# Kernel optimization log

Measured on AMD Instinct MI355X. Metric: run time of the kernel, lower is better.

Reference implementation:

```python
import jax, jax.numpy as jnp
import numpy as np


def setup_inputs() -> dict:
    key = jax.random.key(0)
    k1, k2, k3, k4, k5 = jax.random.split(key, 5)
    B, S, H, L = 32, 4096, 512, 2
    scale = 1.0 / np.sqrt(H)
    return {
        "out": jax.random.normal(k1, (B, S, H), dtype=jnp.float32),
        "hidden": jax.random.normal(k2, (L, B, H), dtype=jnp.float32),
        "W": jax.random.normal(k3, (H, H), dtype=jnp.float32) * scale,
        "b": jax.random.normal(k4, (H,), dtype=jnp.float32) * scale,
        "v": jax.random.normal(k5, (H,), dtype=jnp.float32) * scale,
    }


def reference(out, hidden, W, b, v):
    # hidden_last: (B, 1, H) from last layer
    h_last = hidden[-1][:, None, :]
    # energy = tanh(out @ W^T + b + h_last)  -> (B, S, H)
    energy = jnp.tanh(jnp.einsum("bsh,oh->bso", out, W) + b + h_last)
    # scores = energy @ v  -> (B, S)
    scores = jnp.einsum("bsh,h->bs", energy, v)
    attn = jax.nn.softmax(scores, axis=-1)
    # context = sum_s attn[b,s] * out[b,s,:]  -> (B, H)
    context = jnp.einsum("bs,bsh->bh", attn, out)
    return (context, attn)
```

## Files before the change

kernel.cpp:

```cpp
#include <hip/hip_runtime.h>
#include <hip/hip_bf16.h>

#define B_ 32
#define S_ 4096
#define H_ 512
#define M_ (B_ * S_)
#define L_ 2

typedef __bf16 bf16;
typedef bf16 bf16x8 __attribute__((ext_vector_type(8)));
typedef bf16 bf16x4 __attribute__((ext_vector_type(4)));
typedef float floatx4 __attribute__((ext_vector_type(4)));

__device__ inline bf16 f2b(float f) { return (bf16)f; }

__device__ inline float fast_tanh(float x) {
    float xc = fminf(15.0f, fmaxf(-15.0f, x));
    float e = __expf(2.0f * xc);
    return (e - 1.0f) * __builtin_amdgcn_rcpf(e + 1.0f);
}

__global__ __launch_bounds__(256) void convert_W(const float* __restrict__ W,
                                                 bf16* __restrict__ Wb) {
    int i = blockIdx.x * 256 + threadIdx.x;
    float4 w = ((const float4*)W)[i];
    bf16x4 p = { f2b(w.x), f2b(w.y), f2b(w.z), f2b(w.w) };
    *(bf16x4*)(Wb + (size_t)i * 4) = p;
}

#define MT 64
#define ASTRIDE 520
#define WSTRIDE 40

__global__ __launch_bounds__(256, 2) void scores_kernel(
    const float* __restrict__ outT,
    const bf16*  __restrict__ Wb,
    const float* __restrict__ bias,
    const float* __restrict__ hidden,
    const float* __restrict__ v,
    float* __restrict__ scores)
{
    __shared__ bf16 Alds[MT * ASTRIDE];
    __shared__ bf16 Wlds[128 * WSTRIDE];

    const int tid   = threadIdx.x;
    const int wave  = tid >> 6;
    const int lane  = tid & 63;
    const int mhalf = wave >> 1;
    const int nhalf = wave & 1;
    const int q     = lane >> 4;
    const int l16   = lane & 15;

    const int m0    = blockIdx.x * MT;
    const int batch = m0 >> 12;

    {
        const float4* src = (const float4*)(outT + (size_t)m0 * H_);
        #pragma unroll 4
        for (int it = 0; it < 32; ++it) {
            int idx = it * 256 + tid;
            int r   = idx >> 7;
            int c4  = idx & 127;
            float4 f = src[idx];
            bf16x4 p = { f2b(f.x), f2b(f.y), f2b(f.z), f2b(f.w) };
            *(bf16x4*)&Alds[r * ASTRIDE + c4 * 4] = p;
        }
    }

    float score_acc[2][4];
    #pragma unroll
    for (int mt = 0; mt < 2; ++mt)
        #pragma unroll
        for (int r = 0; r < 4; ++r) score_acc[mt][r] = 0.0f;

    const int nwbase = nhalf * 64;

    for (int nb = 0; nb < 4; ++nb) {
        floatx4 acc[2][4];
        #pragma unroll
        for (int mt = 0; mt < 2; ++mt)
            #pragma unroll
            for (int nt = 0; nt < 4; ++nt)
                acc[mt][nt] = (floatx4){0.f, 0.f, 0.f, 0.f};

        for (int kc = 0; kc < 16; ++kc) {
            __syncthreads();
            {
                int r    = tid >> 1;
                int hcol = tid & 1;
                const bf16* gsrc = Wb + (size_t)(nb * 128 + r) * H_ + kc * 32 + hcol * 16;
                uint4 u0 = *(const uint4*)(gsrc);
                uint4 u1 = *(const uint4*)(gsrc + 8);
                bf16* dst = &Wlds[r * WSTRIDE + hcol * 16];
                *(uint4*)(dst)     = u0;
                *(uint4*)(dst + 8) = u1;
            }
            __syncthreads();

            bf16x8 afrag[2], bfrag[4];
            const int kin = kc * 32 + q * 8;
            #pragma unroll
            for (int mt = 0; mt < 2; ++mt)
                afrag[mt] = *(const bf16x8*)&Alds[(mhalf * 32 + mt * 16 + l16) * ASTRIDE + kin];
            #pragma unroll
            for (int nt = 0; nt < 4; ++nt)
                bfrag[nt] = *(const bf16x8*)&Wlds[(nwbase + nt * 16 + l16) * WSTRIDE + q * 8];
            #pragma unroll
            for (int mt = 0; mt < 2; ++mt)
                #pragma unroll
                for (int nt = 0; nt < 4; ++nt)
                    acc[mt][nt] = __builtin_amdgcn_mfma_f32_16x16x32_bf16(
                        afrag[mt], bfrag[nt], acc[mt][nt], 0, 0, 0);
        }

        #pragma unroll
        for (int nt = 0; nt < 4; ++nt) {
            int n = nb * 128 + nwbase + nt * 16 + l16;
            float bias_n = bias[n] + hidden[(size_t)((L_ - 1) * B_ + batch) * H_ + n];
            float v_n = v[n];
            #pragma unroll
            for (int mt = 0; mt < 2; ++mt)
                #pragma unroll
                for (int r = 0; r < 4; ++r) {
                    float e = fast_tanh(acc[mt][nt][r] + bias_n);
                    score_acc[mt][r] += e * v_n;
                }
        }
    }

    #pragma unroll
    for (int mt = 0; mt < 2; ++mt)
        #pragma unroll
        for (int r = 0; r < 4; ++r) {
            float s = score_acc[mt][r];
            s += __shfl_xor(s, 1);
            s += __shfl_xor(s, 2);
            s += __shfl_xor(s, 4);
            s += __shfl_xor(s, 8);
            score_acc[mt][r] = s;
        }
    if (l16 == 0) {
        #pragma unroll
        for (int mt = 0; mt < 2; ++mt)
            #pragma unroll
            for (int r = 0; r < 4; ++r) {
                int row = m0 + mhalf * 32 + mt * 16 + q * 4 + r;
                atomicAdd(&scores[row], score_acc[mt][r]);
            }
    }
}

__global__ __launch_bounds__(256) void softmax_kernel(const float* __restrict__ scores,
                                                      float* __restrict__ attn) {
    __shared__ float red[4];
    int b = blockIdx.x, tid = threadIdx.x;
    const float* row = scores + (size_t)b * S_;
    float vals[16];
    float mx = -3.4e38f;
    #pragma unroll
    for (int i = 0; i < 16; ++i) { vals[i] = row[i * 256 + tid]; mx = fmaxf(mx, vals[i]); }
    #pragma unroll
    for (int off = 32; off >= 1; off >>= 1) mx = fmaxf(mx, __shfl_xor(mx, off));
    if ((tid & 63) == 0) red[tid >> 6] = mx;
    __syncthreads();
    mx = fmaxf(fmaxf(red[0], red[1]), fmaxf(red[2], red[3]));
    __syncthreads();
    float sum = 0.f;
    #pragma unroll
    for (int i = 0; i < 16; ++i) { vals[i] = __expf(vals[i] - mx); sum += vals[i]; }
    #pragma unroll
    for (int off = 32; off >= 1; off >>= 1) sum += __shfl_xor(sum, off);
    if ((tid & 63) == 0) red[tid >> 6] = sum;
    __syncthreads();
    float inv = 1.0f / (red[0] + red[1] + red[2] + red[3]);
    #pragma unroll
    for (int i = 0; i < 16; ++i) attn[(size_t)b * S_ + i * 256 + tid] = vals[i] * inv;
}

#define SCHUNK 128
__global__ __launch_bounds__(256) void context_kernel(const float* __restrict__ outT,
                                                      const float* __restrict__ attn,
                                                      float* __restrict__ ctx) {
    int b   = blockIdx.y;
    int s0  = blockIdx.x * SCHUNK;
    int tid = threadIdx.x;
    float2 acc = {0.f, 0.f};
    const float2* base = (const float2*)(outT + ((size_t)b * S_ + s0) * H_);
    const float*  arow = attn + (size_t)b * S_ + s0;
    #pragma unroll 4
    for (int s = 0; s < SCHUNK; ++s) {
        float a  = arow[s];
        float2 o = base[(size_t)s * 256 + tid];
        acc.x += a * o.x;
        acc.y += a * o.y;
    }
    float* c = ctx + (size_t)b * H_ + tid * 2;
    atomicAdd(c, acc.x);
    atomicAdd(c + 1, acc.y);
}

extern "C" void kernel_launch(void* const* d_in, const int* in_sizes, int n_in,
                              void* d_out, int out_size, void* d_ws, size_t ws_size,
                              hipStream_t stream) {
    const float* outT   = (const float*)d_in[0];
    const float* hidden = (const float*)d_in[1];
    const float* W      = (const float*)d_in[2];
    const float* bias   = (const float*)d_in[3];
    const float* v      = (const float*)d_in[4];

    float* ctx    = (float*)d_out;
    float* attn   = (float*)d_out + B_ * H_;
    float* scores = (float*)d_ws;
    bf16*  Wb     = (bf16*)((char*)d_ws + (size_t)M_ * sizeof(float));

    hipMemsetAsync(scores, 0, (size_t)M_ * sizeof(float), stream);
    hipMemsetAsync(ctx, 0, (size_t)B_ * H_ * sizeof(float), stream);

    convert_W<<<H_ * H_ / 4 / 256, 256, 0, stream>>>(W, Wb);
    scores_kernel<<<M_ / MT, 256, 0, stream>>>(outT, Wb, bias, hidden, v, scores);
    softmax_kernel<<<B_, 256, 0, stream>>>(scores, attn);
    context_kernel<<<dim3(S_ / SCHUNK, B_), 256, 0, stream>>>(outT, attn, ctx);
}
```

Before: 544.6 us.

## Drop W LDS staging, load W fragments from global, swizzle A tile, widen context loads

The scores kernel no longer stages W through LDS with two barriers per k-chunk. Each wave now takes a 64-column slice of N across all 64 rows and reads W fragments straight from global memory, relying on the cache to hold the small bf16 W. The A tile uses an XOR swizzle in place of padding, and the MFMA tile per wave grows to 4x4, which raises register pressure. The context kernel moves to float4 loads, larger S chunks and two S-groups per block, cutting the number of blocks and atomics.

Measured after the change: 678.3 us. 1.25x slower.

```diff
diff --git a/kernel.cpp b/kernel.cpp
--- a/kernel.cpp
+++ b/kernel.cpp
@@ -29,8 +29,6 @@
 }
 
 #define MT 64
-#define ASTRIDE 520
-#define WSTRIDE 40
 
 __global__ __launch_bounds__(256, 2) void scores_kernel(
     const float* __restrict__ outT,
@@ -40,73 +38,65 @@
     const float* __restrict__ v,
     float* __restrict__ scores)
 {
-    __shared__ bf16 Alds[MT * ASTRIDE];
-    __shared__ bf16 Wlds[128 * WSTRIDE];
-
-    const int tid   = threadIdx.x;
-    const int wave  = tid >> 6;
-    const int lane  = tid & 63;
-    const int mhalf = wave >> 1;
-    const int nhalf = wave & 1;
-    const int q     = lane >> 4;
-    const int l16   = lane & 15;
+    __shared__ bf16 Alds[MT * 512];
+
+    const int tid  = threadIdx.x;
+    const int wave = tid >> 6;
+    const int lane = tid & 63;
+    const int q    = lane >> 4;
+    const int l16  = lane & 15;
 
     const int m0    = blockIdx.x * MT;
     const int batch = m0 >> 12;
 
     {
         const float4* src = (const float4*)(outT + (size_t)m0 * H_);
-        #pragma unroll 4
-        for (int it = 0; it < 32; ++it) {
+        #pragma unroll
+        for (int it = 0; it < 16; ++it) {
             int idx = it * 256 + tid;
-            int r   = idx >> 7;
-            int c4  = idx & 127;
-            float4 f = src[idx];
-            bf16x4 p = { f2b(f.x), f2b(f.y), f2b(f.z), f2b(f.w) };
-            *(bf16x4*)&Alds[r * ASTRIDE + c4 * 4] = p;
+            int r   = idx >> 6;
+            int j   = idx & 63;
+            float4 f0 = src[idx * 2];
+            float4 f1 = src[idx * 2 + 1];
+            bf16x8 p = { f2b(f0.x), f2b(f0.y), f2b(f0.z), f2b(f0.w),
+                         f2b(f1.x), f2b(f1.y), f2b(f1.z), f2b(f1.w) };
+            *(bf16x8*)&Alds[r * 512 + 8 * (j ^ (r & 7))] = p;
         }
     }
-
-    float score_acc[2][4];
-    #pragma unroll
-    for (int mt = 0; mt < 2; ++mt)
+    __syncthreads();
+
+    float score_acc[4][4];
+    #pragma unroll
+    for (int mt = 0; mt < 4; ++mt)
         #pragma unroll
         for (int r = 0; r < 4; ++r) score_acc[mt][r] = 0.0f;
 
-    const int nwbase = nhalf * 64;
-
-    for (int nb = 0; nb < 4; ++nb) {
-        floatx4 acc[2][4];
-        #pragma unroll
-        for (int mt = 0; mt < 2; ++mt)
+    #pragma unroll 1
+    for (int nb = 0; nb < 2; ++nb) {
+        const int nbase = nb * 256 + wave * 64;
+
+        floatx4 acc[4][4];
+        #pragma unroll
+        for (int mt = 0; mt < 4; ++mt)
             #pragma unroll
             for (int nt = 0; nt < 4; ++nt)
                 acc[mt][nt] = (floatx4){0.f, 0.f, 0.f, 0.f};
 
+        #pragma unroll
         for (int kc = 0; kc < 16; ++kc) {
-            __syncthreads();
-            {
-                int r    = tid >> 1;
-                int hcol = tid & 1;
-                const bf16* gsrc = Wb + (size_t)(nb * 128 + r) * H_ + kc * 32 + hcol * 16;
-                uint4 u0 = *(const uint4*)(gsrc);
-                uint4 u1 = *(const uint4*)(gsrc + 8);
-                bf16* dst = &Wlds[r * WSTRIDE + hcol * 16];
-                *(uint4*)(dst)     = u0;
-                *(uint4*)(dst + 8) = u1;
+            bf16x8 bfrag[4], afrag[4];
+            #pragma unroll
+            for (int nt = 0; nt < 4; ++nt)
+                bfrag[nt] = *(const bf16x8*)(Wb + (size_t)(nbase + nt * 16 + l16) * H_
+                                             + kc * 32 + q * 8);
+            const int blk = kc * 4 + q;
+            #pragma unroll
+            for (int mt = 0; mt < 4; ++mt) {
+                int row = mt * 16 + l16;
+                afrag[mt] = *(const bf16x8*)&Alds[row * 512 + 8 * (blk ^ (row & 7))];
             }
-            __syncthreads();
-
-            bf16x8 afrag[2], bfrag[4];
-            const int kin = kc * 32 + q * 8;
-            #pragma unroll
-            for (int mt = 0; mt < 2; ++mt)
-                afrag[mt] = *(const bf16x8*)&Alds[(mhalf * 32 + mt * 16 + l16) * ASTRIDE + kin];
-            #pragma unroll
-            for (int nt = 0; nt < 4; ++nt)
-                bfrag[nt] = *(const bf16x8*)&Wlds[(nwbase + nt * 16 + l16) * WSTRIDE + q * 8];
-            #pragma unroll
-            for (int mt = 0; mt < 2; ++mt)
+            #pragma unroll
+            for (int mt = 0; mt < 4; ++mt)
                 #pragma unroll
                 for (int nt = 0; nt < 4; ++nt)
                     acc[mt][nt] = __builtin_amdgcn_mfma_f32_16x16x32_bf16(
@@ -115,11 +105,11 @@
 
         #pragma unroll
         for (int nt = 0; nt < 4; ++nt) {
-            int n = nb * 128 + nwbase + nt * 16 + l16;
+            int n = nbase + nt * 16 + l16;
             float bias_n = bias[n] + hidden[(size_t)((L_ - 1) * B_ + batch) * H_ + n];
             float v_n = v[n];
             #pragma unroll
-            for (int mt = 0; mt < 2; ++mt)
+            for (int mt = 0; mt < 4; ++mt)
                 #pragma unroll
                 for (int r = 0; r < 4; ++r) {
                     float e = fast_tanh(acc[mt][nt][r] + bias_n);
@@ -129,7 +119,7 @@
     }
 
     #pragma unroll
-    for (int mt = 0; mt < 2; ++mt)
+    for (int mt = 0; mt < 4; ++mt)
         #pragma unroll
         for (int r = 0; r < 4; ++r) {
             float s = score_acc[mt][r];
@@ -137,17 +127,9 @@
             s += __shfl_xor(s, 2);
             s += __shfl_xor(s, 4);
             s += __shfl_xor(s, 8);
-            score_acc[mt][r] = s;
-        }
-    if (l16 == 0) {
-        #pragma unroll
-        for (int mt = 0; mt < 2; ++mt)
-            #pragma unroll
-            for (int r = 0; r < 4; ++r) {
-                int row = m0 + mhalf * 32 + mt * 16 + q * 4 + r;
-                atomicAdd(&scores[row], score_acc[mt][r]);
-            }
-    }
+            if (l16 == 0)
+                atomicAdd(&scores[m0 + mt * 16 + q * 4 + r], s);
+        }
 }
 
 __global__ __launch_bounds__(256) void softmax_kernel(const float* __restrict__ scores,
@@ -177,26 +159,31 @@
     for (int i = 0; i < 16; ++i) attn[(size_t)b * S_ + i * 256 + tid] = vals[i] * inv;
 }
 
-#define SCHUNK 128
-__global__ __launch_bounds__(256) void context_kernel(const float* __restrict__ outT,
-                                                      const float* __restrict__ attn,
-                                                      float* __restrict__ ctx) {
+#define SCHUNK 256
+__global__ __launch_bounds__(256, 2) void context_kernel(const float* __restrict__ outT,
+                                                         const float* __restrict__ attn,
+                                                         float* __restrict__ ctx) {
     int b   = blockIdx.y;
     int s0  = blockIdx.x * SCHUNK;
     int tid = threadIdx.x;
-    float2 acc = {0.f, 0.f};
-    const float2* base = (const float2*)(outT + ((size_t)b * S_ + s0) * H_);
-    const float*  arow = attn + (size_t)b * S_ + s0;
+    int h4  = tid & 127;
+    int sg  = tid >> 7;
+
+    floatx4 acc = {0.f, 0.f, 0.f, 0.f};
+    const floatx4* base = (const floatx4*)(outT + ((size_t)b * S_ + s0) * H_);
+    const float*   arow = attn + (size_t)b * S_ + s0;
+
     #pragma unroll 4
-    for (int s = 0; s < SCHUNK; ++s) {
-        float a  = arow[s];
-        float2 o = base[(size_t)s * 256 + tid];
-        acc.x += a * o.x;
-        acc.y += a * o.y;
+    for (int s = sg; s < SCHUNK; s += 2) {
+        float a   = arow[s];
+        floatx4 o = base[(size_t)s * 128 + h4];
+        acc += a * o;
     }
-    float* c = ctx + (size_t)b * H_ + tid * 2;
-    atomicAdd(c, acc.x);
-    atomicAdd(c + 1, acc.y);
+    float* c = ctx + (size_t)b * H_ + h4 * 4;
+    atomicAdd(c + 0, acc[0]);
+    atomicAdd(c + 1, acc[1]);
+    atomicAdd(c + 2, acc[2]);
+    atomicAdd(c + 3, acc[3]);
 }
 
 extern "C" void kernel_launch(void* const* d_in, const int* in_sizes, int n_in,
```
